# Kernel optimization log

Hardware: AMD Instinct MI355X
Metric: run time of the kernel (lower is better)

Reference implementation:

```python
import math
import jax, jax.numpy as jnp
import numpy as np

D_MODEL = 896
N_HEADS = 14
D_HEAD = D_MODEL // N_HEADS  # 64
ROPE_BASE = 10000.0
LN_EPS = 1e-5
B, N = 8, 1024


def setup_inputs() -> dict:
    key = jax.random.key(0)
    ks = jax.random.split(key, 12)
    s = 1.0 / math.sqrt(D_MODEL)
    return {
        "node_features": jax.random.normal(ks[0], (B, N, D_MODEL), jnp.float32),
        "adj": jax.random.uniform(ks[1], (N, N), jnp.float32),
        "wind_dirs": jax.random.uniform(ks[2], (B, N), jnp.float32),
        "bearings": jax.random.uniform(ks[3], (N, N), jnp.float32),
        "Wq": jax.random.normal(ks[4], (D_MODEL, D_MODEL), jnp.float32) * s,
        "Wk": jax.random.normal(ks[5], (D_MODEL, D_MODEL), jnp.float32) * s,
        "Wv": jax.random.normal(ks[6], (D_MODEL, D_MODEL), jnp.float32) * s,
        "Wo": jax.random.normal(ks[7], (D_MODEL, D_MODEL), jnp.float32) * s,
        "ln_g": jnp.ones((D_MODEL,), jnp.float32),
        "ln_b": jnp.zeros((D_MODEL,), jnp.float32),
        "wind_w": jax.random.normal(ks[8], (2, N_HEADS), jnp.float32) * (1.0 / math.sqrt(2.0)),
        "wind_b": jnp.zeros((N_HEADS,), jnp.float32),
    }


def _layernorm(x, g, b):
    mu = jnp.mean(x, axis=-1, keepdims=True)
    var = jnp.var(x, axis=-1, keepdims=True)
    return (x - mu) * jax.lax.rsqrt(var + LN_EPS) * g + b


def _apply_rotary(x, cos_h, sin_h):
    # x: (B,H,N,d_head); cos_h/sin_h: (N, d_head//2)
    d_half = x.shape[-1] // 2
    x1, x2 = x[..., :d_half], x[..., d_half:]
    return jnp.concatenate([x1 * cos_h - x2 * sin_h, x2 * cos_h + x1 * sin_h], axis=-1)


def reference(node_features, adj, wind_dirs, bearings, Wq, Wk, Wv, Wo, ln_g, ln_b, wind_w, wind_b):
    Bb, Nn, D = node_features.shape
    residual = node_features
    x = _layernorm(node_features, ln_g, ln_b)

    def proj(W):
        return (x @ W).reshape(Bb, Nn, N_HEADS, D_HEAD).transpose(0, 2, 1, 3)  # (B,H,N,dh)

    Q, K, V = proj(Wq), proj(Wk), proj(Wv)

    # RoPE: cos/sin halves (first d_half entries of the duplicated freq table)
    inv_freq = 1.0 / (ROPE_BASE ** (jnp.arange(0, D_HEAD, 2, dtype=jnp.float32) / D_HEAD))
    freqs = jnp.arange(Nn, dtype=jnp.float32)[:, None] * inv_freq[None, :]  # (N, dh/2)
    cos_h, sin_h = jnp.cos(freqs), jnp.sin(freqs)
    Q = _apply_rotary(Q, cos_h, sin_h)
    K = _apply_rotary(K, cos_h, sin_h)

    attn = jnp.einsum("bhqd,bhkd->bhqk", Q, K) / math.sqrt(D_HEAD)
    adj_mask = (adj > 0)[None, None, :, :]
    attn = jnp.where(adj_mask, attn, -1e30)

    # wind-direction dynamic edge bias
    reverse_bearings = (bearings.T + 180.0) % 360.0  # (N,N)
    alignment = jnp.cos(jnp.deg2rad(wind_dirs[:, :, None] - reverse_bearings[None]))  # (B,N,N)
    dist_feat = jnp.broadcast_to(adj[None], (Bb, Nn, Nn))
    edge_features = jnp.stack([alignment, dist_feat], axis=-1)  # (B,N,N,2)
    wind_bias = jnp.tanh(edge_features @ wind_w + wind_b)  # (B,N,N,H)
    attn = attn + wind_bias.transpose(0, 3, 1, 2)  # (B,H,N,N)

    attn = jax.nn.softmax(attn, axis=-1)  # dropout is identity in eval
    out = jnp.einsum("bhqk,bhkd->bhqd", attn, V)
    out = out.transpose(0, 2, 1, 3).reshape(Bb, Nn, D) @ Wo
    return residual + out
```

## Files before the change

### kernel.cpp

```cpp
#include <hip/hip_runtime.h>
#include <hip/hip_bf16.h>
#include <math.h>

#define B_ 8
#define N_ 1024
#define H_ 14
#define DH_ 64
#define D_ 896
#define M_ (B_*N_)
#define DQKV_ 2688

#define TWO_LOG2E_ 2.8853900817779268f
#define BIAS_C_   (-15.869645449778597f)
#define QSCALE_     0.18033688011112043f

typedef __attribute__((ext_vector_type(8))) short bf16x8;
typedef __attribute__((ext_vector_type(4))) short bf16x4;
typedef __attribute__((ext_vector_type(4))) float f32x4;
typedef __attribute__((ext_vector_type(4))) unsigned u32x4;

__device__ __forceinline__ float bf2f(short s){
  unsigned u = ((unsigned)(unsigned short)s) << 16;
  union { unsigned u; float f; } c; c.u = u; return c.f;
}
__device__ __forceinline__ short f2bf(float f){
  union { float f; unsigned u; } c; c.f = f;
  unsigned u = c.u;
  unsigned r = (u + 0x7FFFu + ((u >> 16) & 1u)) >> 16;
  return (short)(unsigned short)r;
}
__device__ __forceinline__ float asf(unsigned u){
  union { unsigned u; float f; } c; c.u = u; return c.f;
}
__device__ __forceinline__ unsigned cvt_pk_bf16(float lo, float hi){
  unsigned r;
  asm("v_cvt_pk_bf16_f32 %0, %1, %2" : "=v"(r) : "v"(lo), "v"(hi));
  return r;
}

#define BAR_LDS() do { asm volatile("s_waitcnt lgkmcnt(0)" ::: "memory"); \
                       __builtin_amdgcn_s_barrier(); } while (0)

__global__ __launch_bounds__(256) void ln_kernel(const float* __restrict__ x,
                                                 const float* __restrict__ g,
                                                 const float* __restrict__ bb,
                                                 short* __restrict__ y)
{
  int row = blockIdx.x;
  const float* xr = x + (size_t)row * D_;
  float s = 0.f, s2 = 0.f;
  for (int i = threadIdx.x; i < D_; i += 256){
    float v = xr[i]; s += v; s2 = fmaf(v, v, s2);
  }
  #pragma unroll
  for (int off = 32; off > 0; off >>= 1){
    s  += __shfl_down(s,  off, 64);
    s2 += __shfl_down(s2, off, 64);
  }
  __shared__ float rs_[4], rs2_[4];
  int wv = threadIdx.x >> 6;
  if ((threadIdx.x & 63) == 0){ rs_[wv] = s; rs2_[wv] = s2; }
  __syncthreads();
  float ts  = rs_[0] + rs_[1] + rs_[2] + rs_[3];
  float ts2 = rs2_[0] + rs2_[1] + rs2_[2] + rs2_[3];
  float mu  = ts * (1.f / D_);
  float var = ts2 * (1.f / D_) - mu * mu;
  float rstd = rsqrtf(var + 1e-5f);
  short* yr = y + (size_t)row * D_;
  for (int i = threadIdx.x; i < D_; i += 256){
    yr[i] = f2bf((xr[i] - mu) * rstd * g[i] + bb[i]);
  }
}

__global__ __launch_bounds__(256) void transpose_kernel(
    const float* __restrict__ Wq, const float* __restrict__ Wk,
    const float* __restrict__ Wv, const float* __restrict__ Wo,
    short* __restrict__ WqkvT, short* __restrict__ WoT)
{
  __shared__ short t[64][72];
  int z = blockIdx.z;
  const float* W = (z == 0) ? Wq : (z == 1) ? Wk : (z == 2) ? Wv : Wo;
  int kb = blockIdx.x * 64, nb = blockIdx.y * 64;
  int c0 = (threadIdx.x & 7) * 8;
  int r0 = threadIdx.x >> 3;
  #pragma unroll
  for (int rr = 0; rr < 64; rr += 32){
    const float* src = &W[(size_t)(kb + r0 + rr) * D_ + nb + c0];
    float4 a = *(const float4*)src;
    float4 b = *(const float4*)(src + 4);
    short* dstl = &t[r0 + rr][c0];
    dstl[0] = f2bf(a.x); dstl[1] = f2bf(a.y); dstl[2] = f2bf(a.z); dstl[3] = f2bf(a.w);
    dstl[4] = f2bf(b.x); dstl[5] = f2bf(b.y); dstl[6] = f2bf(b.z); dstl[7] = f2bf(b.w);
  }
  __syncthreads();
  short* dst = (z < 3) ? (WqkvT + (size_t)(z * D_) * D_) : WoT;
  #pragma unroll
  for (int rr = 0; rr < 64; rr += 32){
    int n = nb + r0 + rr;
    bf16x8 v;
    #pragma unroll
    for (int j = 0; j < 8; j++) v[j] = t[c0 + j][r0 + rr];
    *(bf16x8*)&dst[(size_t)n * D_ + kb + c0] = v;
  }
}

__global__ __launch_bounds__(256) void prep_kernel(
    const float* __restrict__ adj, const float* __restrict__ brg,
    const float* __restrict__ wdir,
    unsigned* __restrict__ csb, short* __restrict__ adjT,
    short* __restrict__ alignT, int do_align)
{
  int kt = blockIdx.x, qt = blockIdx.y;
  __shared__ short tt[64][72];
  __shared__ float cA_[8][64], sA_[8][64];

  if (do_align){
    for (int idx = threadIdx.x; idx < 8 * 64; idx += 256){
      int b = idx >> 6, q = idx & 63;
      float A = wdir[(size_t)b * N_ + qt * 64 + q] * 0.017453292519943295f;
      float s, c; __sincosf(A, &s, &c);
      sA_[b][q] = s; cA_[b][q] = c;
    }
  }

  int r  = threadIdx.x >> 2;
  int c0 = (threadIdx.x & 3) * 16;

  {
    int q = qt * 64 + r;
    const float* ap = adj + (size_t)q * N_ + kt * 64 + c0;
    #pragma unroll
    for (int i = 0; i < 16; i += 4){
      float4 av = *(const float4*)(ap + i);
      tt[r][c0 + i]     = f2bf(av.x);
      tt[r][c0 + i + 1] = f2bf(av.y);
      tt[r][c0 + i + 2] = f2bf(av.z);
      tt[r][c0 + i + 3] = f2bf(av.w);
    }
  }
  __syncthreads();

  {
    int k = kt * 64 + r;
    const float* bp = brg + (size_t)k * N_ + qt * 64 + c0;
    unsigned* cp = csb + (size_t)k * N_ + qt * 64 + c0;
    #pragma unroll
    for (int i = 0; i < 16; i += 4){
      float4 bv = *(const float4*)(bp + i);
      float b4[4] = { bv.x, bv.y, bv.z, bv.w };
      float cB[4], sB[4];
      unsigned o[4];
      #pragma unroll
      for (int j = 0; j < 4; j++){
        float Br = (b4[j] + 180.f) * 0.017453292519943295f;
        __sincosf(Br, &sB[j], &cB[j]);
        o[j] = ((unsigned)(unsigned short)f2bf(cB[j])) |
               (((unsigned)(unsigned short)f2bf(sB[j])) << 16);
      }
      *(uint4*)(cp + i) = make_uint4(o[0], o[1], o[2], o[3]);
      if (do_align){
        #pragma unroll
        for (int b = 0; b < 8; b++){
          unsigned w2[2];
          #pragma unroll
          for (int p = 0; p < 2; p++){
            unsigned lo = 0, hi = 0;
            #pragma unroll
            for (int j = 0; j < 2; j++){
              int q = c0 + i + p * 2 + j;
              float al = fmaf(cA_[b][q], cB[p * 2 + j], sA_[b][q] * sB[p * 2 + j]);
              unsigned v = (unsigned)(unsigned short)f2bf(al);
              if (j == 0) lo = v; else hi = v;
            }
            w2[p] = lo | (hi << 16);
          }
          *(uint2*)(alignT + ((size_t)b * N_ + k) * N_ + qt * 64 + c0 + i) =
              make_uint2(w2[0], w2[1]);
        }
      }
    }
  }

  {
    int k = kt * 64 + r;
    short* op = adjT + (size_t)k * N_ + qt * 64 + c0;
    bf16x8 v0, v1;
    #pragma unroll
    for (int j = 0; j < 8; j++){ v0[j] = tt[c0 + j][r]; v1[j] = tt[c0 + 8 + j][r]; }
    *(bf16x8*)op = v0;
    *(bf16x8*)(op + 8) = v1;
  }
}

__global__ __launch_bounds__(256) void gemm_bt(const short* __restrict__ A,
                                               const short* __restrict__ Bt,
                                               short* __restrict__ C,
                                               float* __restrict__ Cf,
                                               const float* __restrict__ residf,
                                               int N, int rope)
{
  const int K = D_;
  __shared__ short As[128 * 32];
  __shared__ short Bs[128 * 32];
  int tid  = threadIdx.x;
  int wave = tid >> 6;
  int lane = tid & 63;
  int quad = lane >> 4;
  int l16  = lane & 15;
  int wr = wave >> 1, wc = wave & 1;
  int m0 = blockIdx.x * 128;
  int n0 = blockIdx.y * 128;

  f32x4 acc[4][4];
  #pragma unroll
  for (int i = 0; i < 4; i++)
    #pragma unroll
    for (int j = 0; j < 4; j++)
      acc[i][j] = (f32x4){0.f, 0.f, 0.f, 0.f};

  for (int k0 = 0; k0 < K; k0 += 32){
    __syncthreads();
    #pragma unroll
    for (int it = 0; it < 2; ++it){
      int c   = tid + it * 256;
      int row = c >> 2;
      int cc  = c & 3;
      const short* ga = A  + (size_t)(m0 + row) * K + k0 + cc * 8;
      const short* gb = Bt + (size_t)(n0 + row) * K + k0 + cc * 8;
      short* la = As + (size_t)(wave * 64 + it * 256) * 8;
      short* lb = Bs + (size_t)(wave * 64 + it * 256) * 8;
      __builtin_amdgcn_global_load_lds((const __attribute__((address_space(1))) void*)ga,
                                       (__attribute__((address_space(3))) void*)la, 16, 0, 0);
      __builtin_amdgcn_global_load_lds((const __attribute__((address_space(1))) void*)gb,
                                       (__attribute__((address_space(3))) void*)lb, 16, 0, 0);
    }
    __syncthreads();

    bf16x8 af[4], bfr[4];
    #pragma unroll
    for (int i = 0; i < 4; i++)
      af[i] = *(const bf16x8*)(As + (size_t)(wr * 64 + i * 16 + l16) * 32 + quad * 8);
    #pragma unroll
    for (int j = 0; j < 4; j++)
      bfr[j] = *(const bf16x8*)(Bs + (size_t)(wc * 64 + j * 16 + l16) * 32 + quad * 8);
    #pragma unroll
    for (int i = 0; i < 4; i++)
      #pragma unroll
      for (int j = 0; j < 4; j++)
        acc[i][j] = __builtin_amdgcn_mfma_f32_16x16x32_bf16(af[i], bfr[j], acc[i][j], 0, 0, 0);
  }

  if (rope){
    int cb  = n0 + wc * 64;
    int mat = cb / D_;
    if (mat < 2){
      float scale = (mat == 0) ? QSCALE_ : 1.0f;
      float invf0 = exp2f(-0.4152410118609203f * (float)l16);
      float invf1 = invf0 * 0.01f;
      #pragma unroll
      for (int i = 0; i < 4; i++){
        #pragma unroll
        for (int rr = 0; rr < 4; rr++){
          int r = m0 + wr * 64 + i * 16 + quad * 4 + rr;
          float nseq = (float)(r & (N_ - 1));
          float s0, c0v, s1, c1v;
          __sincosf(nseq * invf0, &s0, &c0v);
          __sincosf(nseq * invf1, &s1, &c1v);
          float x1 = acc[i][0][rr], x2 = acc[i][2][rr];
          acc[i][0][rr] = (x1 * c0v - x2 * s0) * scale;
          acc[i][2][rr] = (x2 * c0v + x1 * s0) * scale;
          x1 = acc[i][1][rr]; x2 = acc[i][3][rr];
          acc[i][1][rr] = (x1 * c1v - x2 * s1) * scale;
          acc[i][3][rr] = (x2 * c1v + x1 * s1) * scale;
        }
      }
    }
  }

  #pragma unroll
  for (int i = 0; i < 4; i++){
    #pragma unroll
    for (int rr = 0; rr < 4; rr++){
      int r = m0 + wr * 64 + i * 16 + quad * 4 + rr;
      size_t rowoff = (size_t)r * N;
      #pragma unroll
      for (int j = 0; j < 4; j++){
        int cidx = n0 + wc * 64 + j * 16 + l16;
        float v = acc[i][j][rr];
        if (Cf){
          Cf[rowoff + cidx] = v + residf[rowoff + cidx];
        } else {
          C[rowoff + cidx] = f2bf(v);
        }
      }
    }
  }
}

template<int PRE>
__global__ __launch_bounds__(512, 4) void attn_kernel(
    const short* __restrict__ QKV,
    const unsigned* __restrict__ csb,
    const short* __restrict__ adjT,
    const short* __restrict__ alignT,
    const float* __restrict__ wind_dirs,
    const float* __restrict__ wind_w,
    const float* __restrict__ wind_b,
    short* __restrict__ outb)
{
  __shared__ short K_s[64 * 72];
  __shared__ short V_t[64 * 76];
  __shared__ short P_s[128 * 76];

  int bid = blockIdx.x;
  int qt  = bid / 112;
  int rem = bid - qt * 112;
  int hh  = rem >> 3;
  int b   = rem & 7;
  int q0  = qt * 128;
  int kt0 = (qt * 2) & 15;

  int t    = threadIdx.x;
  int w    = t >> 6;
  int lane = t & 63;
  int quad = lane >> 4;
  int l16  = lane & 15;

  const short* qp = QKV + ((size_t)(b * N_) + q0 + w * 16 + l16) * DQKV_ + hh * DH_;
  bf16x8 qf0 = *(const bf16x8*)(qp + quad * 8);
  bf16x8 qf1 = *(const bf16x8*)(qp + 32 + quad * 8);

  float cA[4], sA[4];
  if (!PRE){
    #pragma unroll
    for (int rr = 0; rr < 4; rr++){
      float wd = wind_dirs[(size_t)b * N_ + q0 + w * 16 + quad * 4 + rr];
      float A  = wd * 0.017453292519943295f;
      sA[rr] = __sinf(A);
      cA[rr] = __cosf(A);
    }
  }
  float w0m = wind_w[hh]      * TWO_LOG2E_;
  float w1m = wind_w[H_ + hh] * TWO_LOG2E_;
  float wbm = wind_b[hh]      * TWO_LOG2E_;

  float l[4] = {0.f, 0.f, 0.f, 0.f};
  f32x4 O[4];
  #pragma unroll
  for (int dc = 0; dc < 4; dc++) O[dc] = (f32x4){0.f, 0.f, 0.f, 0.f};

  int kr  = t >> 3, kc8 = (t & 7) * 8;
  int vk2 = (t >> 4) * 2, vd4 = (t & 15) * 4;
  const short* kg0 = QKV + ((size_t)(b * N_) + kr)  * DQKV_ + D_     + hh * DH_ + kc8;
  const short* vg0 = QKV + ((size_t)(b * N_) + vk2) * DQKV_ + 2 * D_ + hh * DH_ + vd4;

  int k0f = kt0 * 64;
  bf16x8 pk  = *(const bf16x8*)(kg0 + (size_t)k0f * DQKV_);
  bf16x4 pv0 = *(const bf16x4*)(vg0 + (size_t)k0f * DQKV_);
  bf16x4 pv1 = *(const bf16x4*)(vg0 + (size_t)(k0f + 1) * DQKV_);

  size_t bias_q = (size_t)(q0 + w * 16 + quad * 4);
  u32x4 cs4a[4]; bf16x4 al4a[4]; bf16x4 av4a[4];
  #pragma unroll
  for (int jc = 0; jc < 4; jc++){
    size_t off = (size_t)(k0f + jc * 16 + l16) * N_ + bias_q;
    if (PRE) al4a[jc] = *(const bf16x4*)(alignT + (size_t)b * N_ * N_ + off);
    else     cs4a[jc] = *(const u32x4*)(csb + off);
    av4a[jc] = *(const bf16x4*)(adjT + off);
  }

  for (int it = 0; it < 16; ++it){
    int ktn = (it + 1 + kt0) & 15;
    int kn  = ktn * 64;

    BAR_LDS();
    *(bf16x8*)(K_s + kr * 72 + kc8) = pk;
    #pragma unroll
    for (int j = 0; j < 4; j++){
      unsigned pv = ((unsigned)(unsigned short)pv0[j]) |
                    (((unsigned)(unsigned short)pv1[j]) << 16);
      *(unsigned*)(V_t + (vd4 + j) * 76 + vk2) = pv;
    }
    BAR_LDS();

    pk  = *(const bf16x8*)(kg0 + (size_t)kn * DQKV_);
    pv0 = *(const bf16x4*)(vg0 + (size_t)kn * DQKV_);
    pv1 = *(const bf16x4*)(vg0 + (size_t)(kn + 1) * DQKV_);

    f32x4 S[4];
    __builtin_amdgcn_s_setprio(1);
    #pragma unroll
    for (int jc = 0; jc < 4; jc++){
      S[jc] = (f32x4){0.f, 0.f, 0.f, 0.f};
      bf16x8 kf0 = *(const bf16x8*)(K_s + (jc * 16 + l16) * 72 + quad * 8);
      bf16x8 kf1 = *(const bf16x8*)(K_s + (jc * 16 + l16) * 72 + 32 + quad * 8);
      S[jc] = __builtin_amdgcn_mfma_f32_16x16x32_bf16(qf0, kf0, S[jc], 0, 0, 0);
      S[jc] = __builtin_amdgcn_mfma_f32_16x16x32_bf16(qf1, kf1, S[jc], 0, 0, 0);
    }
    __builtin_amdgcn_s_setprio(0);

    #pragma unroll
    for (int kc = 0; kc < 2; kc++){
      #pragma unroll
      for (int jc = kc * 2; jc < kc * 2 + 2; jc++){
        float ev[4];
        #pragma unroll
        for (int rr = 0; rr < 4; rr++){
          float av = bf2f(av4a[jc][rr]);
          float align;
          if (PRE){
            align = bf2f(al4a[jc][rr]);
          } else {
            unsigned u = cs4a[jc][rr];
            float cB = asf(u << 16);
            float sB = asf(u & 0xffff0000u);
            align = cA[rr] * cB + sA[rr] * sB;
          }
          float z2 = fmaf(align, w0m, fmaf(av, w1m, wbm));
          float e2 = __builtin_amdgcn_exp2f(z2);
          float rc = __builtin_amdgcn_rcpf(e2 + 1.f);
          float bias2 = fmaf(-TWO_LOG2E_, rc, BIAS_C_);
          float sv = (av > 0.f ? S[jc][rr] : -1e30f) + bias2;
          float e = __builtin_amdgcn_exp2f(sv);
          l[rr] += e;
          ev[rr] = e;
        }
        unsigned pk01 = cvt_pk_bf16(ev[0], ev[1]);
        unsigned pk23 = cvt_pk_bf16(ev[2], ev[3]);
        short* pb = P_s + (w * 16 + quad * 4) * 76 + jc * 16 + l16;
        pb[0]   = (short)pk01;
        pb[76]  = (short)(pk01 >> 16);
        pb[152] = (short)pk23;
        pb[228] = (short)(pk23 >> 16);
      }

      __builtin_amdgcn_s_setprio(1);
      {
        const short* pp = P_s + (w * 16 + l16) * 76 + kc * 32 + quad * 8;
        bf16x4 p0 = *(const bf16x4*)pp;
        bf16x4 p1 = *(const bf16x4*)(pp + 4);
        bf16x8 pf = { p0[0], p0[1], p0[2], p0[3], p1[0], p1[1], p1[2], p1[3] };
        #pragma unroll
        for (int dc = 0; dc < 4; dc++){
          const short* vp = V_t + (dc * 16 + l16) * 76 + kc * 32 + quad * 8;
          bf16x4 u0 = *(const bf16x4*)vp;
          bf16x4 u1 = *(const bf16x4*)(vp + 4);
          bf16x8 vf = { u0[0], u0[1], u0[2], u0[3], u1[0], u1[1], u1[2], u1[3] };
          O[dc] = __builtin_amdgcn_mfma_f32_16x16x32_bf16(pf, vf, O[dc], 0, 0, 0);
        }
      }
      __builtin_amdgcn_s_setprio(0);

      #pragma unroll
      for (int jc = kc * 2; jc < kc * 2 + 2; jc++){
        size_t off = (size_t)(kn + jc * 16 + l16) * N_ + bias_q;
        if (PRE) al4a[jc] = *(const bf16x4*)(alignT + (size_t)b * N_ * N_ + off);
        else     cs4a[jc] = *(const u32x4*)(csb + off);
        av4a[jc] = *(const bf16x4*)(adjT + off);
      }
    }
  }

  float rl[4];
  #pragma unroll
  for (int rr = 0; rr < 4; rr++){
    float rs = l[rr];
    rs += __shfl_xor(rs, 1);
    rs += __shfl_xor(rs, 2);
    rs += __shfl_xor(rs, 4);
    rs += __shfl_xor(rs, 8);
    rl[rr] = 1.f / rs;
  }
  short* op = outb + ((size_t)(b * N_) + q0 + w * 16) * D_ + hh * DH_;
  #pragma unroll
  for (int rr = 0; rr < 4; rr++)
    #pragma unroll
    for (int dc = 0; dc < 4; dc++)
      op[(size_t)(quad * 4 + rr) * D_ + dc * 16 + l16] = f2bf(O[dc][rr] * rl[rr]);
}

extern "C" void kernel_launch(void* const* d_in, const int* in_sizes, int n_in,
                              void* d_out, int out_size, void* d_ws, size_t ws_size,
                              hipStream_t stream)
{
  const float* nf   = (const float*)d_in[0];
  const float* adj  = (const float*)d_in[1];
  const float* wdir = (const float*)d_in[2];
  const float* brg  = (const float*)d_in[3];
  const float* Wq   = (const float*)d_in[4];
  const float* Wk   = (const float*)d_in[5];
  const float* Wv   = (const float*)d_in[6];
  const float* Wo   = (const float*)d_in[7];
  const float* lng  = (const float*)d_in[8];
  const float* lnb  = (const float*)d_in[9];
  const float* ww   = (const float*)d_in[10];
  const float* wbb  = (const float*)d_in[11];
  float* out = (float*)d_out;

  short* base = (short*)d_ws;
  size_t sh = 0;
  short* xln   = base + sh;  sh += (size_t)M_ * D_;
  short* WqkvT = base + sh;  sh += (size_t)DQKV_ * D_;
  short* WoT   = base + sh;  sh += (size_t)D_ * D_;
  short* QKV   = base + sh;  sh += (size_t)M_ * DQKV_;
  unsigned* csb = (unsigned*)(base + sh); sh += (size_t)N_ * N_ * 2;
  short* adjT  = base + sh;  sh += (size_t)N_ * N_;
  short* alignT = base + sh; sh += (size_t)B_ * N_ * N_;
  size_t need_pre = sh * sizeof(short);
  bool pre = (ws_size >= need_pre);

  ln_kernel<<<M_, 256, 0, stream>>>(nf, lng, lnb, xln);
  transpose_kernel<<<dim3(14, 14, 4), 256, 0, stream>>>(Wq, Wk, Wv, Wo, WqkvT, WoT);
  prep_kernel<<<dim3(16, 16), 256, 0, stream>>>(adj, brg, wdir, csb, adjT, alignT, pre ? 1 : 0);
  gemm_bt<<<dim3(M_ / 128, DQKV_ / 128), 256, 0, stream>>>(xln, WqkvT, QKV, nullptr, nullptr, DQKV_, 1);
  if (pre)
    attn_kernel<1><<<B_ * H_ * 8, 512, 0, stream>>>(QKV, csb, adjT, alignT, wdir, ww, wbb, xln);
  else
    attn_kernel<0><<<B_ * H_ * 8, 512, 0, stream>>>(QKV, csb, adjT, alignT, wdir, ww, wbb, xln);
  gemm_bt<<<dim3(M_ / 128, D_ / 128), 256, 0, stream>>>(xln, WoT, nullptr, out, nf, D_, 0);
}
```

Baseline: 384.4 us.

## Halve attention query tile to 64 rows and restructure prep alignment stores

Measured after the change: 371.3 us. 3.4% less time.

```diff
diff --git a/kernel.cpp b/kernel.cpp
--- a/kernel.cpp
+++ b/kernel.cpp
@@ -140,49 +140,51 @@
   }
   __syncthreads();
 
+  int k = kt * 64 + r;
+  float cB[16], sB[16];
   {
-    int k = kt * 64 + r;
     const float* bp = brg + (size_t)k * N_ + qt * 64 + c0;
-    unsigned* cp = csb + (size_t)k * N_ + qt * 64 + c0;
     #pragma unroll
     for (int i = 0; i < 16; i += 4){
       float4 bv = *(const float4*)(bp + i);
       float b4[4] = { bv.x, bv.y, bv.z, bv.w };
-      float cB[4], sB[4];
-      unsigned o[4];
       #pragma unroll
       for (int j = 0; j < 4; j++){
         float Br = (b4[j] + 180.f) * 0.017453292519943295f;
-        __sincosf(Br, &sB[j], &cB[j]);
-        o[j] = ((unsigned)(unsigned short)f2bf(cB[j])) |
-               (((unsigned)(unsigned short)f2bf(sB[j])) << 16);
-      }
+        __sincosf(Br, &sB[i + j], &cB[i + j]);
+      }
+    }
+  }
+
+  if (do_align){
+    #pragma unroll
+    for (int b = 0; b < 8; b++){
+      unsigned w8[8];
+      #pragma unroll
+      for (int p = 0; p < 8; p++){
+        int q0i = c0 + 2 * p, q1i = q0i + 1;
+        float a0 = fmaf(cA_[b][q0i], cB[2 * p],     sA_[b][q0i] * sB[2 * p]);
+        float a1 = fmaf(cA_[b][q1i], cB[2 * p + 1], sA_[b][q1i] * sB[2 * p + 1]);
+        w8[p] = cvt_pk_bf16(a0, a1);
+      }
+      short* dst = alignT + ((size_t)b * N_ + k) * N_ + qt * 64 + c0;
+      *(uint4*)dst       = make_uint4(w8[0], w8[1], w8[2], w8[3]);
+      *(uint4*)(dst + 8) = make_uint4(w8[4], w8[5], w8[6], w8[7]);
+    }
+  } else {
+    unsigned* cp = csb + (size_t)k * N_ + qt * 64 + c0;
+    #pragma unroll
+    for (int i = 0; i < 16; i += 4){
+      unsigned o[4];
+      #pragma unroll
+      for (int j = 0; j < 4; j++)
+        o[j] = ((unsigned)(unsigned short)f2bf(cB[i + j])) |
+               (((unsigned)(unsigned short)f2bf(sB[i + j])) << 16);
       *(uint4*)(cp + i) = make_uint4(o[0], o[1], o[2], o[3]);
-      if (do_align){
-        #pragma unroll
-        for (int b = 0; b < 8; b++){
-          unsigned w2[2];
-          #pragma unroll
-          for (int p = 0; p < 2; p++){
-            unsigned lo = 0, hi = 0;
-            #pragma unroll
-            for (int j = 0; j < 2; j++){
-              int q = c0 + i + p * 2 + j;
-              float al = fmaf(cA_[b][q], cB[p * 2 + j], sA_[b][q] * sB[p * 2 + j]);
-              unsigned v = (unsigned)(unsigned short)f2bf(al);
-              if (j == 0) lo = v; else hi = v;
-            }
-            w2[p] = lo | (hi << 16);
-          }
-          *(uint2*)(alignT + ((size_t)b * N_ + k) * N_ + qt * 64 + c0 + i) =
-              make_uint2(w2[0], w2[1]);
-        }
-      }
     }
   }
 
   {
-    int k = kt * 64 + r;
     short* op = adjT + (size_t)k * N_ + qt * 64 + c0;
     bf16x8 v0, v1;
     #pragma unroll
@@ -298,7 +300,7 @@
 }
 
 template<int PRE>
-__global__ __launch_bounds__(512, 4) void attn_kernel(
+__global__ __launch_bounds__(256, 4) void attn_kernel(
     const short* __restrict__ QKV,
     const unsigned* __restrict__ csb,
     const short* __restrict__ adjT,
@@ -310,15 +312,15 @@
 {
   __shared__ short K_s[64 * 72];
   __shared__ short V_t[64 * 76];
-  __shared__ short P_s[128 * 76];
+  __shared__ short P_s[64 * 76];
 
   int bid = blockIdx.x;
   int qt  = bid / 112;
   int rem = bid - qt * 112;
   int hh  = rem >> 3;
   int b   = rem & 7;
-  int q0  = qt * 128;
-  int kt0 = (qt * 2) & 15;
+  int q0  = qt * 64;
+  int kt0 = qt;
 
   int t    = threadIdx.x;
   int w    = t >> 6;
@@ -349,15 +351,18 @@
   #pragma unroll
   for (int dc = 0; dc < 4; dc++) O[dc] = (f32x4){0.f, 0.f, 0.f, 0.f};
 
-  int kr  = t >> 3, kc8 = (t & 7) * 8;
-  int vk2 = (t >> 4) * 2, vd4 = (t & 15) * 4;
-  const short* kg0 = QKV + ((size_t)(b * N_) + kr)  * DQKV_ + D_     + hh * DH_ + kc8;
-  const short* vg0 = QKV + ((size_t)(b * N_) + vk2) * DQKV_ + 2 * D_ + hh * DH_ + vd4;
+  int kr   = t >> 2, kc16 = (t & 3) * 16;
+  int vk4  = (t >> 4) * 4, vd4 = (t & 15) * 4;
+  const short* kg0 = QKV + ((size_t)(b * N_) + kr)  * DQKV_ + D_     + hh * DH_ + kc16;
+  const short* vg0 = QKV + ((size_t)(b * N_) + vk4) * DQKV_ + 2 * D_ + hh * DH_ + vd4;
 
   int k0f = kt0 * 64;
-  bf16x8 pk  = *(const bf16x8*)(kg0 + (size_t)k0f * DQKV_);
-  bf16x4 pv0 = *(const bf16x4*)(vg0 + (size_t)k0f * DQKV_);
+  bf16x8 pk0 = *(const bf16x8*)(kg0 + (size_t)k0f * DQKV_);
+  bf16x8 pk1 = *(const bf16x8*)(kg0 + (size_t)k0f * DQKV_ + 8);
+  bf16x4 pv0 = *(const bf16x4*)(vg0 + (size_t)(k0f + 0) * DQKV_);
   bf16x4 pv1 = *(const bf16x4*)(vg0 + (size_t)(k0f + 1) * DQKV_);
+  bf16x4 pv2 = *(const bf16x4*)(vg0 + (size_t)(k0f + 2) * DQKV_);
+  bf16x4 pv3 = *(const bf16x4*)(vg0 + (size_t)(k0f + 3) * DQKV_);
 
   size_t bias_q = (size_t)(q0 + w * 16 + quad * 4);
   u32x4 cs4a[4]; bf16x4 al4a[4]; bf16x4 av4a[4];
@@ -374,18 +379,24 @@
     int kn  = ktn * 64;
 
     BAR_LDS();
-    *(bf16x8*)(K_s + kr * 72 + kc8) = pk;
+    *(bf16x8*)(K_s + kr * 72 + kc16)     = pk0;
+    *(bf16x8*)(K_s + kr * 72 + kc16 + 8) = pk1;
     #pragma unroll
     for (int j = 0; j < 4; j++){
-      unsigned pv = ((unsigned)(unsigned short)pv0[j]) |
+      unsigned lo = ((unsigned)(unsigned short)pv0[j]) |
                     (((unsigned)(unsigned short)pv1[j]) << 16);
-      *(unsigned*)(V_t + (vd4 + j) * 76 + vk2) = pv;
+      unsigned hi = ((unsigned)(unsigned short)pv2[j]) |
+                    (((unsigned)(unsigned short)pv3[j]) << 16);
+      *(uint2*)(V_t + (vd4 + j) * 76 + vk4) = make_uint2(lo, hi);
     }
     BAR_LDS();
 
-    pk  = *(const bf16x8*)(kg0 + (size_t)kn * DQKV_);
-    pv0 = *(const bf16x4*)(vg0 + (size_t)kn * DQKV_);
+    pk0 = *(const bf16x8*)(kg0 + (size_t)kn * DQKV_);
+    pk1 = *(const bf16x8*)(kg0 + (size_t)kn * DQKV_ + 8);
+    pv0 = *(const bf16x4*)(vg0 + (size_t)(kn + 0) * DQKV_);
     pv1 = *(const bf16x4*)(vg0 + (size_t)(kn + 1) * DQKV_);
+    pv2 = *(const bf16x4*)(vg0 + (size_t)(kn + 2) * DQKV_);
+    pv3 = *(const bf16x4*)(vg0 + (size_t)(kn + 3) * DQKV_);
 
     f32x4 S[4];
     __builtin_amdgcn_s_setprio(1);
@@ -514,8 +525,8 @@
   prep_kernel<<<dim3(16, 16), 256, 0, stream>>>(adj, brg, wdir, csb, adjT, alignT, pre ? 1 : 0);
   gemm_bt<<<dim3(M_ / 128, DQKV_ / 128), 256, 0, stream>>>(xln, WqkvT, QKV, nullptr, nullptr, DQKV_, 1);
   if (pre)
-    attn_kernel<1><<<B_ * H_ * 8, 512, 0, stream>>>(QKV, csb, adjT, alignT, wdir, ww, wbb, xln);
+    attn_kernel<1><<<B_ * H_ * 16, 256, 0, stream>>>(QKV, csb, adjT, alignT, wdir, ww, wbb, xln);
   else
-    attn_kernel<0><<<B_ * H_ * 8, 512, 0, stream>>>(QKV, csb, adjT, alignT, wdir, ww, wbb, xln);
+    attn_kernel<0><<<B_ * H_ * 16, 256, 0, stream>>>(QKV, csb, adjT, alignT, wdir, ww, wbb, xln);
   gemm_bt<<<dim3(M_ / 128, D_ / 128), 256, 0, stream>>>(xln, WoT, nullptr, out, nf, D_, 0);
 }
```
